# Optimization experiments

Hardware: AMD Instinct MI355X
Metric: run time of the kernel (lower is better)

## Reference

```python
import jax, jax.numpy as jnp
import numpy as np

D = 1024      # d_model
H = 16        # n_heads
HD = D // H   # head_dim = 64
B = 2
T = 2048


def setup_inputs() -> dict:
    key = jax.random.key(0)
    k0, k1, k2 = jax.random.split(key, 3)
    s = 1.0 / np.sqrt(D)
    return {
        "x": jax.random.normal(k0, (B, T, D), dtype=jnp.float32),
        "qkv_w": jax.random.normal(k1, (D, 3 * D), dtype=jnp.float32) * s,
        "qkv_b": jnp.zeros((3 * D,), dtype=jnp.float32),
        "out_w": jax.random.normal(k2, (D, D), dtype=jnp.float32) * s,
        "out_b": jnp.zeros((D,), dtype=jnp.float32),
    }


def _apply_rotary(x, rope):
    # Faithful to the torch apply_rotary: even/odd interleaved split of both
    # x and the [sin(freqs)|cos(freqs)] rope table.
    x1, x2 = x[..., ::2], x[..., 1::2]
    sin, cos = rope[..., ::2], rope[..., 1::2]
    return jnp.concatenate([x1 * cos - x2 * sin, x1 * sin + x2 * cos], axis=-1)


def reference(x, qkv_w, qkv_b, out_w, out_b):
    Bx, Tx, Dm = x.shape
    # QKV projection -> [3, B, H, T, HD]
    qkv = (x @ qkv_w + qkv_b).reshape(Bx, Tx, 3, H, HD).transpose(2, 0, 3, 1, 4)
    q, k, v = qkv[0], qkv[1], qkv[2]

    # Rotary table: rope = concat(sin(freqs), cos(freqs)) along last dim -> [T, HD]
    inv_freq = 1.0 / (10000.0 ** (jnp.arange(0, HD, 2, dtype=jnp.float32) / HD))
    t = jnp.arange(Tx, dtype=jnp.float32)
    freqs = t[:, None] * inv_freq[None, :]          # [T, HD/2]
    rope = jnp.concatenate([jnp.sin(freqs), jnp.cos(freqs)], axis=-1)  # [T, HD]

    q = _apply_rotary(q, rope)
    k = _apply_rotary(k, rope)

    scale = HD ** -0.5
    scores = jnp.einsum('bhqd,bhkd->bhqk', q, k) * scale  # [B,H,T,T]
    causal_mask = jnp.triu(jnp.ones((Tx, Tx), dtype=bool), 1)
    scores = jnp.where(causal_mask, -jnp.inf, scores)
    attn = jax.nn.softmax(scores, axis=-1)
    # dropout is identity in eval mode
    out = jnp.einsum('bhqk,bhkd->bhqd', attn, v)           # [B,H,T,HD]
    out = out.transpose(0, 2, 1, 3).reshape(Bx, Tx, Dm)    # [B,T,D]
    return out @ out_w + out_b
```

## Files before the change

### kernel.cpp

```cpp
#include <hip/hip_runtime.h>

typedef unsigned short u16;
typedef __attribute__((ext_vector_type(8))) __bf16 bf16x8;
typedef __attribute__((ext_vector_type(4))) float f32x4;

#define NB 2
#define NT 2048
#define ND 1024
#define NH 16
#define HD 64

__device__ __forceinline__ float b2f(u16 u) {
  union { float f; unsigned int i; } v; v.i = ((unsigned int)u) << 16; return v.f;
}
__device__ __forceinline__ u16 f2b(float f) {
  union { float f; unsigned int i; } v; v.f = f;
  unsigned int r = (v.i + 0x7FFFu + ((v.i >> 16) & 1u)) >> 16;
  return (u16)r;
}
__device__ __forceinline__ unsigned int cvtpk(float lo, float hi) {
  unsigned int pk;
  asm("v_cvt_pk_bf16_f32 %0, %1, %2" : "=v"(pk) : "v"(lo), "v"(hi));
  return pk;
}

__device__ __forceinline__ void gload_lds16(const u16* g, u16* lds) {
  __builtin_amdgcn_global_load_lds(
      (const __attribute__((address_space(1))) unsigned int*)(g),
      (__attribute__((address_space(3))) unsigned int*)(lds),
      16, 0, 0);
}

__device__ __forceinline__ f32x4 mfma16(bf16x8 a, bf16x8 b, f32x4 c) {
  return __builtin_amdgcn_mfma_f32_16x16x32_bf16(a, b, c, 0, 0, 0);
}

template <int N>
__device__ __forceinline__ float ror16(float x) {
  return __int_as_float(__builtin_amdgcn_update_dpp(
      __float_as_int(x), __float_as_int(x), 0x120 | N, 0xF, 0xF, true));
}
__device__ __forceinline__ float rsum16(float x) {
  x += ror16<8>(x);
  x += ror16<4>(x);
  x += ror16<2>(x);
  x += ror16<1>(x);
  return x;
}

__device__ __forceinline__ float fast_sin(float a) {
  float r = a * 0.15915494309189535f;
  r -= floorf(r);
  return __builtin_amdgcn_sinf(r);
}
__device__ __forceinline__ float fast_cos(float a) {
  float r = a * 0.15915494309189535f;
  r -= floorf(r);
  return __builtin_amdgcn_cosf(r);
}

__global__ __launch_bounds__(256) void prep_inputs(
    const float* __restrict__ x, const float* __restrict__ qkv_w,
    const float* __restrict__ out_w, u16* __restrict__ xb,
    u16* __restrict__ wqkvT, u16* __restrict__ woutT,
    float* __restrict__ rtab) {
  __shared__ u16 tile[32][33];
  const int blk = blockIdx.x;
  const int tid = threadIdx.x;
  if (blk < 2048) {
    int i = (blk * 256 + tid) * 8;
#pragma unroll
    for (int j = 0; j < 8; ++j) xb[i + j] = f2b(x[i + j]);
    return;
  }
  if (blk >= 6144) {
    const float LOG1E4 = 9.210340371976184f;
    int base = (blk - 6144) * 4096 + tid * 16;
#pragma unroll
    for (int j = 0; j < 16; ++j) {
      int idx = base + j;
      int t = idx >> 6, c = idx & 63;
      float inv = __expf(-((float)(c & 31)) * (1.0f / 32.0f) * LOG1E4);
      float a = (float)t * inv;
      rtab[idx] = (c < 32) ? fast_sin(a) : fast_cos(a);
    }
    return;
  }
  const float* in; u16* out; int N; int idx;
  if (blk < 5120) { idx = blk - 2048; in = qkv_w; out = wqkvT; N = 3072; }
  else            { idx = blk - 5120; in = out_w; out = woutT; N = 1024; }
  const int nbx = N / 32;
  const int n0 = (idx % nbx) * 32, k0 = (idx / nbx) * 32;
  const int tx = tid & 31, ty = tid >> 5;
  for (int i2 = ty; i2 < 32; i2 += 8)
    tile[i2][tx] = f2b(in[(size_t)(k0 + i2) * N + n0 + tx]);
  __syncthreads();
  for (int i2 = ty; i2 < 32; i2 += 8)
    out[(size_t)(n0 + i2) * 1024 + k0 + tx] = tile[tx][i2];
}

__global__ __launch_bounds__(256, 3) void gemm64_2ph(const u16* __restrict__ A,
                                                     const u16* __restrict__ Bt,
                                                     const float* __restrict__ bias,
                                                     float* __restrict__ C,
                                                     int M, int N, int K) {
  __shared__ alignas(16) u16 As[2][4096];
  __shared__ alignas(16) u16 Bs[2][8192];
  const int tid = threadIdx.x;
  const int lane = tid & 63;
  const int wave = tid >> 6;
  const int l15 = lane & 15, quad = lane >> 4;
  const int wm = (wave >> 1) * 32, wn = (wave & 1) * 64;

  const int lin = blockIdx.y * gridDim.x + blockIdx.x;
  const int xcd = lin & 7, loc = lin >> 3;
  const int row0 = (xcd * 8 + (loc >> 3)) * 64;
  const int col0 = (loc & 7) * 128;

  const int sr = tid >> 3;
  const size_t soff = (size_t)sr * K + (size_t)((tid & 7) ^ (sr & 7)) * 8;
  const u16* Ab = A + (size_t)row0 * K;
  const u16* Bb = Bt + (size_t)col0 * K;

  const int swz0 = (quad ^ (l15 & 7)) * 8;
  const int swz1 = ((4 + quad) ^ (l15 & 7)) * 8;
  const int arow = (wm + l15) * 64;
  const int brow = (wn + l15) * 64;

  f32x4 acc[2][4] = {};
  const int NTIL = K >> 6;

#define STAGEA(buf, koff)                                                    \
  _Pragma("unroll") for (int p = 0; p < 2; ++p)                              \
      gload_lds16(Ab + (koff) + soff + (size_t)p * 32 * K,                   \
                  &As[buf][(p * 256 + tid) * 8]);
#define STAGEB(buf, koff)                                                    \
  _Pragma("unroll") for (int p = 0; p < 4; ++p)                              \
      gload_lds16(Bb + (koff) + soff + (size_t)p * 32 * K,                   \
                  &Bs[buf][(p * 256 + tid) * 8]);

  STAGEA(0, 0);
  STAGEB(0, 0);
  asm volatile("s_waitcnt vmcnt(0)");
  __builtin_amdgcn_s_barrier();
  asm volatile("" ::: "memory");

  for (int t = 0; t < NTIL; ++t) {
    const int cur = t & 1;
    if (t + 1 < NTIL) {
      STAGEA(cur ^ 1, (size_t)(t + 1) * 64);
      STAGEB(cur ^ 1, (size_t)(t + 1) * 64);
    }
    bf16x8 af[2][2], bfr[4][2];
#pragma unroll
    for (int i = 0; i < 2; ++i) {
      af[i][0] = *(const bf16x8*)&As[cur][arow + i * 1024 + swz0];
      af[i][1] = *(const bf16x8*)&As[cur][arow + i * 1024 + swz1];
    }
#pragma unroll
    for (int j = 0; j < 4; ++j) {
      bfr[j][0] = *(const bf16x8*)&Bs[cur][brow + j * 1024 + swz0];
      bfr[j][1] = *(const bf16x8*)&Bs[cur][brow + j * 1024 + swz1];
    }
    asm volatile("s_waitcnt lgkmcnt(0)");
    __builtin_amdgcn_sched_barrier(0);
#pragma unroll
    for (int i = 0; i < 2; ++i)
#pragma unroll
      for (int j = 0; j < 4; ++j) {
        acc[i][j] = mfma16(af[i][0], bfr[j][0], acc[i][j]);
        acc[i][j] = mfma16(af[i][1], bfr[j][1], acc[i][j]);
      }
    asm volatile("s_waitcnt vmcnt(0)");
    __builtin_amdgcn_s_barrier();
    asm volatile("" ::: "memory");
  }
#undef STAGEA
#undef STAGEB

#pragma unroll
  for (int j = 0; j < 4; ++j) {
    const int c = col0 + wn + j * 16 + l15;
    const float bv = bias[c];
#pragma unroll
    for (int i = 0; i < 2; ++i) {
      const int rr0 = row0 + wm + i * 16 + quad * 4;
      f32x4 v = acc[i][j];
#pragma unroll
      for (int rr = 0; rr < 4; ++rr)
        C[(size_t)(rr0 + rr) * N + c] = v[rr] + bv;
    }
  }
}

__device__ __forceinline__ void stage2(const u16* g0, const u16* g1, u16* l,
                                       int tid) {
  gload_lds16(g0, &l[tid * 8]);
  gload_lds16(g1, &l[(512 + tid) * 8]);
}

__device__ __forceinline__ u16* tsw(u16* base, int row, int col) {
  int byte = row * 512 + ((col * 2) ^ ((row & 15) << 4));
  return (u16*)((char*)base + byte);
}

#define AH(b, h) (&lds[((b) * 2 + (h)) * 8192])
#define BH(b, h) (&lds[32768 + ((b) * 2 + (h)) * 8192])

#define LOAD_AFX(dst, base)                                                 \
  _Pragma("unroll") for (int mm = 0; mm < 4; ++mm) {                        \
    dst[mm][0] = *(const bf16x8*)&(base)[arow + mm * 2048 + swz0];          \
    dst[mm][1] = *(const bf16x8*)&(base)[arow + mm * 2048 + swz1];          \
  }
#define LOAD_BF(base)                                                       \
  _Pragma("unroll") for (int nn = 0; nn < 2; ++nn) {                        \
    bfr[nn][0] = *(const bf16x8*)&(base)[brow + nn * 4096 + swz0];          \
    bfr[nn][1] = *(const bf16x8*)&(base)[brow + nn * 4096 + swz1];          \
  }
#define MFMA_QX(afv, MA, NQ)                                                \
  _Pragma("unroll") for (int mm = 0; mm < 4; ++mm)                          \
  _Pragma("unroll") for (int nn = 0; nn < 2; ++nn) {                        \
    acc[(MA) * 4 + mm][(NQ) * 2 + nn] =                                     \
        mfma16(afv[mm][0], bfr[nn][0], acc[(MA) * 4 + mm][(NQ) * 2 + nn]);  \
    acc[(MA) * 4 + mm][(NQ) * 2 + nn] =                                     \
        mfma16(afv[mm][1], bfr[nn][1], acc[(MA) * 4 + mm][(NQ) * 2 + nn]);  \
  }
#define PH_SYNC                                                             \
  __builtin_amdgcn_s_barrier();                                             \
  asm volatile("s_waitcnt lgkmcnt(0)");                                     \
  __builtin_amdgcn_sched_barrier(0);                                        \
  __builtin_amdgcn_s_setprio(1);
#define PH_END                                                              \
  __builtin_amdgcn_s_setprio(0);                                            \
  __builtin_amdgcn_s_barrier();                                             \
  asm volatile("" ::: "memory");

__global__ __launch_bounds__(512, 2) void gemm256_qkv(const u16* __restrict__ A,
                                                      const u16* __restrict__ Bt,
                                                      const float* __restrict__ bias,
                                                      u16* __restrict__ qsw,
                                                      u16* __restrict__ ksw,
                                                      u16* __restrict__ vsw,
                                                      const float* __restrict__ rope_tab,
                                                      int K) {
  __shared__ alignas(16) u16 lds[65536];
  const int tid = threadIdx.x;
  const int lane = tid & 63;
  const int wave = tid >> 6;
  const int l15 = lane & 15, quad = lane >> 4;
  const int wm = wave >> 2, wn = wave & 3;

  const int lin = blockIdx.y * gridDim.x + blockIdx.x;
  const int xcd = lin & 7, loc = lin >> 3;
  const int row0 = ((xcd & 3) * 4 + loc / 6) * 256;
  const int col0 = ((xcd >> 2) * 6 + loc % 6) * 256;
  const int NTIL = K >> 6;

  const int sr = tid >> 3;
  const size_t soff = (size_t)sr * K + (size_t)((tid & 7) ^ (sr & 7)) * 8;
  const size_t hK = (size_t)64 * K;
  const u16* A0p = A + (size_t)row0 * K + soff;
  const u16* A1p = A0p + 2 * hK;
  const u16* B0p = Bt + (size_t)col0 * K + soff;
  const u16* B1p = B0p + 2 * hK;

  const int swz0 = (quad ^ (l15 & 7)) * 8;
  const int swz1 = ((4 + quad) ^ (l15 & 7)) * 8;
  const int arow = (wm * 16 + l15) * 64;
  const int brow = (wn * 16 + l15) * 64;

  f32x4 acc[8][4] = {};

  stage2(B0p, B0p + hK, BH(0, 0), tid);
  stage2(A1p, A1p + hK, AH(0, 1), tid);
  stage2(A0p, A0p + hK, AH(0, 0), tid);
  stage2(B1p, B1p + hK, BH(0, 1), tid);
  {
    int tp = (NTIL > 1) ? 1 : 0;
    stage2(B0p + tp * 64, B0p + tp * 64 + hK, BH(1, 0), tid);
    stage2(A1p + tp * 64, A1p + tp * 64 + hK, AH(1, 1), tid);
  }
  asm volatile("s_waitcnt vmcnt(4)");
  __builtin_amdgcn_s_barrier();
  asm volatile("" ::: "memory");

  bf16x8 afA[4][2], afB[4][2], bfr[2][2];
#pragma unroll 2
  for (int t = 0; t < NTIL; ++t) {
    const int cur = t & 1, nxt = cur ^ 1;
    const int o1 = ((t + 1 < NTIL) ? t + 1 : NTIL - 1) * 64;
    const int o2 = ((t + 2 < NTIL) ? t + 2 : NTIL - 1) * 64;
    u16* Ac0 = AH(cur, 0);
    u16* Ac1 = AH(cur, 1);
    u16* Bc0 = BH(cur, 0);
    u16* Bc1 = BH(cur, 1);

    LOAD_AFX(afA, Ac0);
    LOAD_BF(Bc0);
    stage2(A0p + o1, A0p + o1 + hK, AH(nxt, 0), tid);
    PH_SYNC; MFMA_QX(afA, 0, 0); PH_END;

    LOAD_AFX(afB, Ac1);
    stage2(B1p + o1, B1p + o1 + hK, BH(nxt, 1), tid);
    PH_SYNC; MFMA_QX(afB, 1, 0); PH_END;

    LOAD_BF(Bc1);
    stage2(B0p + o2, B0p + o2 + hK, Bc0, tid);
    PH_SYNC; MFMA_QX(afB, 1, 1); PH_END;

    stage2(A1p + o2, A1p + o2 + hK, Ac1, tid);
    __builtin_amdgcn_s_barrier();
    __builtin_amdgcn_sched_barrier(0);
    __builtin_amdgcn_s_setprio(1);
    MFMA_QX(afA, 0, 1);
    __builtin_amdgcn_s_setprio(0);
    asm volatile("s_waitcnt vmcnt(4)");
    __builtin_amdgcn_s_barrier();
    asm volatile("" ::: "memory");
  }
  asm volatile("s_waitcnt vmcnt(0)");
  __syncthreads();

#pragma unroll
  for (int ni = 0; ni < 4; ++ni) {
    const int col_in = (ni >> 1) * 128 + (ni & 1) * 64 + wn * 16 + l15;
    const float bv = bias[col0 + col_in];
#pragma unroll
    for (int mi = 0; mi < 8; ++mi) {
      const int r_in0 = (mi >> 2) * 128 + (mi & 3) * 32 + wm * 16 + quad * 4;
      f32x4 v = acc[mi][ni];
#pragma unroll
      for (int rr = 0; rr < 4; ++rr)
        *tsw(lds, r_in0 + rr, col_in) = f2b(v[rr] + bv);
    }
  }
  __syncthreads();

  const int tt = col0 >> 10;
  const int h0 = (col0 & 1023) >> 6;
  const int bb = row0 >> 11;
  const int tb0 = row0 & 2047;

  if (tt < 2) {
    u16* dst = (tt == 0) ? qsw : ksw;
    const float scale = (tt == 0) ? 0.125f : 1.0f;
    const int hh = tid >> 7;
    const int chunk = (tid >> 4) & 7;
    const int tl = tid & 15;
    const int ks = chunk >> 2, qd = chunk & 3;
    const int bh = bb * 16 + h0 + hh;
    const bool low = (ks == 0);
    const int cbase = qd * 16;
    const int xbyte0 = (hh * 64 + cbase) * 2;
    const int sw = tl << 4;
    for (int tb = 0; tb < 8; ++tb) {
      const int tbt = tb0 + tb * 32;
#pragma unroll
      for (int rbloc = 0; rbloc < 2; ++rbloc) {
        const int rrow = tb * 32 + rbloc * 16 + tl;
        const int tg = tbt + rbloc * 16 + tl;
        const char* rowp = (const char*)lds + rrow * 512;
        bf16x8 q0 = *(const bf16x8*)(rowp + (xbyte0 ^ sw));
        bf16x8 q1 = *(const bf16x8*)(rowp + ((xbyte0 + 16) ^ sw));
        const float* tp = &rope_tab[tg * 64 + cbase];
        float sc[16];
        *(f32x4*)&sc[0]  = *(const f32x4*)(tp);
        *(f32x4*)&sc[4]  = *(const f32x4*)(tp + 4);
        *(f32x4*)&sc[8]  = *(const f32x4*)(tp + 8);
        *(f32x4*)&sc[12] = *(const f32x4*)(tp + 12);
        u16 xs[16];
        *(bf16x8*)&xs[0] = q0;
        *(bf16x8*)&xs[8] = q1;
        union { u16 s[8]; unsigned int u[4]; bf16x8 v; } o;
        float ovv[8];
#pragma unroll
        for (int e = 0; e < 8; ++e) {
          float x1 = b2f(xs[2 * e]), x2 = b2f(xs[2 * e + 1]);
          float sA = sc[2 * e], cA = sc[2 * e + 1];
          float ov = low ? (x1 * cA - x2 * sA) : (x1 * sA + x2 * cA);
          ovv[e] = ov * scale;
        }
#pragma unroll
        for (int p2 = 0; p2 < 4; ++p2)
          o.u[p2] = cvtpk(ovv[2 * p2], ovv[2 * p2 + 1]);
        size_t addr =
            ((((size_t)bh * 128 + (tbt >> 4) + rbloc) * 2 + ks) * 64 +
             qd * 16 + tl) * 8;
        *(bf16x8*)&dst[addr] = o.v;
      }
    }
  } else {
    const int u = tid >> 8;
    const int utid = tid & 255;
    const int ni = utid >> 6, lane2 = utid & 63;
    const int qd = lane2 >> 4, l15b = lane2 & 15;
    for (int it = 0; it < 16; ++it) {
      const int unit = it * 2 + u;
      const int hh = unit >> 3, tb = unit & 7;
      const int bh = bb * 16 + h0 + hh;
      const int tbt = tb0 + tb * 32;
      union { u16 s[8]; bf16x8 v; } o;
#pragma unroll
      for (int e = 0; e < 8; ++e) {
        int p = qd * 8 + e;
        int krow = (p >> 1) + ((p & 1) << 4);
        o.s[e] = *tsw(lds, tb * 32 + krow, hh * 64 + ni * 16 + l15b);
      }
      *(bf16x8*)&vsw[(((size_t)bh * 64 + (tbt >> 5)) * 4 + ni) * 512 +
                     lane2 * 8] = o.v;
    }
  }
}

__global__ __launch_bounds__(128, 2) void flash_kernel(const u16* __restrict__ qsw,
                                                       const u16* __restrict__ ksw,
                                                       const u16* __restrict__ vsw,
                                                       u16* __restrict__ attn) {
  __shared__ alignas(16) u16 Ps[2 * 5120];
  float* const Of = (float*)&Ps[5120];
  float* const Ll = (float*)&Ps[9216];

  const int tid = threadIdx.x;
  const int w = tid >> 6;
  const int lane = tid & 63;
  const int l15 = lane & 15, quad = lane >> 4;
  const int linear = (int)blockIdx.x;
  const int bh = linear & 31;
  const int qt = 63 - (linear >> 5);
  const int r0 = qt * 32;
  u16* Psw = &Ps[w * 5120];

  bf16x8 aq[2][2];
#pragma unroll
  for (int mi = 0; mi < 2; ++mi)
#pragma unroll
    for (int ks = 0; ks < 2; ++ks)
      aq[mi][ks] = *(const bf16x8*)&qsw[
          ((((size_t)bh * 128 + qt * 2 + mi) * 2 + ks) * 64 + lane) * 8];

  f32x4 oacc[2][4] = {};
  float lst[8] = {0.f, 0.f, 0.f, 0.f, 0.f, 0.f, 0.f, 0.f};

  const int ktmax = qt >> 2;
  for (int kt = w; kt <= ktmax; kt += 2) {
    bf16x8 kf[2][8];
#pragma unroll
    for (int ks = 0; ks < 2; ++ks)
#pragma unroll
      for (int ni = 0; ni < 8; ++ni)
        kf[ks][ni] = *(const bf16x8*)&ksw[
            ((((size_t)bh * 128 + kt * 8 + ni) * 2 + ks) * 64 + lane) * 8];

    f32x4 sacc[2][8] = {};
#pragma unroll
    for (int ks = 0; ks < 2; ++ks)
#pragma unroll
      for (int ni = 0; ni < 8; ++ni) {
        sacc[0][ni] = mfma16(aq[0][ks], kf[ks][ni], sacc[0][ni]);
        sacc[1][ni] = mfma16(aq[1][ks], kf[ks][ni], sacc[1][ni]);
      }

    bf16x8 vf[4][4];
#pragma unroll
    for (int ks = 0; ks < 4; ++ks)
#pragma unroll
      for (int ni = 0; ni < 4; ++ni)
        vf[ks][ni] = *(const bf16x8*)&vsw[
            (((size_t)bh * 64 + kt * 4 + ks) * 4 + ni) * 512 + lane * 8];

    const bool diag = (kt == ktmax);
    const int k0 = kt * 128;
#pragma unroll
    for (int mi = 0; mi < 2; ++mi)
#pragma unroll
      for (int r = 0; r < 4; ++r) {
        const int prow = mi * 16 + quad * 4 + r;
        float sv[8];
#pragma unroll
        for (int ni = 0; ni < 8; ++ni) sv[ni] = sacc[mi][ni][r];
        if (diag) {
#pragma unroll
          for (int ni = 0; ni < 8; ++ni)
            if (k0 + ni * 16 + l15 > r0 + prow) sv[ni] = -__builtin_inff();
        }
        float rs = 0.f;
#pragma unroll
        for (int ni = 0; ni < 8; ++ni) {
          float p = __expf(sv[ni]);
          sv[ni] = p;
          rs += p;
        }
        lst[mi * 4 + r] += rsum16(rs);
#pragma unroll
        for (int ni = 0; ni < 8; ni += 2) {
          unsigned int pk = cvtpk(sv[ni], sv[ni + 1]);
          *(unsigned int*)&Psw[(ni >> 1) * 1280 + prow * 40 + 2 * l15] = pk;
        }
      }

    asm volatile("" ::: "memory");

#pragma unroll
    for (int ks = 0; ks < 4; ++ks) {
      bf16x8 ap0 = *(const bf16x8*)&Psw[ks * 1280 + l15 * 40 + quad * 8];
      bf16x8 ap1 = *(const bf16x8*)&Psw[ks * 1280 + (16 + l15) * 40 + quad * 8];
#pragma unroll
      for (int ni = 0; ni < 4; ++ni) {
        oacc[0][ni] = mfma16(ap0, vf[ks][ni], oacc[0][ni]);
        oacc[1][ni] = mfma16(ap1, vf[ks][ni], oacc[1][ni]);
      }
    }
  }

  if (w == 1) {
#pragma unroll
    for (int mi = 0; mi < 2; ++mi)
#pragma unroll
      for (int r = 0; r < 4; ++r) {
        const int row = mi * 16 + quad * 4 + r;
        if (l15 == 0) Ll[row] = lst[mi * 4 + r];
#pragma unroll
        for (int ni = 0; ni < 4; ++ni)
          Of[row * 64 + ni * 16 + l15] = oacc[mi][ni][r];
      }
  }
  __syncthreads();
  if (w == 0) {
    const int b = bh >> 4, h = bh & 15;
#pragma unroll
    for (int mi = 0; mi < 2; ++mi)
#pragma unroll
      for (int r = 0; r < 4; ++r) {
        const int row = mi * 16 + quad * 4 + r;
        const float rl = 1.0f / (lst[mi * 4 + r] + Ll[row]);
        const int trow = r0 + row;
#pragma unroll
        for (int ni = 0; ni < 4; ++ni) {
          float o = oacc[mi][ni][r] + Of[row * 64 + ni * 16 + l15];
          attn[((size_t)b * NT + trow) * ND + h * HD + ni * 16 + l15] = f2b(o * rl);
        }
      }
  }
}

extern "C" void kernel_launch(void* const* d_in, const int* in_sizes, int n_in,
                              void* d_out, int out_size, void* d_ws, size_t ws_size,
                              hipStream_t stream) {
  const float* x = (const float*)d_in[0];
  const float* qkv_w = (const float*)d_in[1];
  const float* qkv_b = (const float*)d_in[2];
  const float* out_w = (const float*)d_in[3];
  const float* out_b = (const float*)d_in[4];
  float* out = (float*)d_out;

  u16* ws = (u16*)d_ws;
  u16* xb    = ws;
  u16* wqkvT = xb + (size_t)4096 * 1024;
  u16* woutT = wqkvT + 3072 * 1024;
  u16* qsw   = woutT + 1024 * 1024;
  u16* ksw   = qsw + (size_t)32 * 2048 * 64;
  u16* vsw   = ksw + (size_t)32 * 2048 * 64;
  u16* attn  = vsw + (size_t)32 * 2048 * 64;
  float* rtab = (float*)(attn + (size_t)4096 * 1024);

  prep_inputs<<<dim3(6176), 256, 0, stream>>>(
      x, qkv_w, out_w, xb, wqkvT, woutT, rtab);

  gemm256_qkv<<<dim3(12, 16), 512, 0, stream>>>(
      xb, wqkvT, qkv_b, qsw, ksw, vsw, rtab, ND);

  flash_kernel<<<dim3(2048), 128, 0, stream>>>(qsw, ksw, vsw, attn);

  gemm64_2ph<<<dim3(ND / 128, NB * NT / 64), 256, 0, stream>>>(
      attn, woutT, out_b, out, NB * NT, ND, ND);
}
```

Measured before the change: 179.0 us.

## Replace 256x256 QKV GEMM with simpler 128x128 double-buffered tile kernel

The QKV projection moves from a 256x256 tile, 512-thread kernel with a hand-staged four-phase pipeline to a 128x128 tile, 256-thread kernel with plain double buffering and a single MFMA block per K-step. The grid grows from 192 to 768 blocks, which fills the 256 CUs more evenly than 192 blocks did. The cost is lower operand reuse per tile, more global and LDS traffic, and less overlap between loads and MFMA because each iteration waits on vmcnt(0). The epilogue's rope and V-scatter loops are resized to the smaller tile.

Result: no change. 181.5 us (+1.4%).

```diff
diff --git a/kernel.cpp b/kernel.cpp
--- a/kernel.cpp
+++ b/kernel.cpp
@@ -193,145 +193,100 @@
   }
 }
 
-__device__ __forceinline__ void stage2(const u16* g0, const u16* g1, u16* l,
-                                       int tid) {
-  gload_lds16(g0, &l[tid * 8]);
-  gload_lds16(g1, &l[(512 + tid) * 8]);
-}
-
-__device__ __forceinline__ u16* tsw(u16* base, int row, int col) {
-  int byte = row * 512 + ((col * 2) ^ ((row & 15) << 4));
+__device__ __forceinline__ u16* tsw128(u16* base, int row, int col) {
+  int byte = row * 256 + ((col * 2) ^ ((row & 15) << 4));
   return (u16*)((char*)base + byte);
 }
 
-#define AH(b, h) (&lds[((b) * 2 + (h)) * 8192])
-#define BH(b, h) (&lds[32768 + ((b) * 2 + (h)) * 8192])
-
-#define LOAD_AFX(dst, base)                                                 \
-  _Pragma("unroll") for (int mm = 0; mm < 4; ++mm) {                        \
-    dst[mm][0] = *(const bf16x8*)&(base)[arow + mm * 2048 + swz0];          \
-    dst[mm][1] = *(const bf16x8*)&(base)[arow + mm * 2048 + swz1];          \
-  }
-#define LOAD_BF(base)                                                       \
-  _Pragma("unroll") for (int nn = 0; nn < 2; ++nn) {                        \
-    bfr[nn][0] = *(const bf16x8*)&(base)[brow + nn * 4096 + swz0];          \
-    bfr[nn][1] = *(const bf16x8*)&(base)[brow + nn * 4096 + swz1];          \
-  }
-#define MFMA_QX(afv, MA, NQ)                                                \
-  _Pragma("unroll") for (int mm = 0; mm < 4; ++mm)                          \
-  _Pragma("unroll") for (int nn = 0; nn < 2; ++nn) {                        \
-    acc[(MA) * 4 + mm][(NQ) * 2 + nn] =                                     \
-        mfma16(afv[mm][0], bfr[nn][0], acc[(MA) * 4 + mm][(NQ) * 2 + nn]);  \
-    acc[(MA) * 4 + mm][(NQ) * 2 + nn] =                                     \
-        mfma16(afv[mm][1], bfr[nn][1], acc[(MA) * 4 + mm][(NQ) * 2 + nn]);  \
-  }
-#define PH_SYNC                                                             \
-  __builtin_amdgcn_s_barrier();                                             \
-  asm volatile("s_waitcnt lgkmcnt(0)");                                     \
-  __builtin_amdgcn_sched_barrier(0);                                        \
-  __builtin_amdgcn_s_setprio(1);
-#define PH_END                                                              \
-  __builtin_amdgcn_s_setprio(0);                                            \
-  __builtin_amdgcn_s_barrier();                                             \
-  asm volatile("" ::: "memory");
-
-__global__ __launch_bounds__(512, 2) void gemm256_qkv(const u16* __restrict__ A,
-                                                      const u16* __restrict__ Bt,
-                                                      const float* __restrict__ bias,
-                                                      u16* __restrict__ qsw,
-                                                      u16* __restrict__ ksw,
-                                                      u16* __restrict__ vsw,
-                                                      const float* __restrict__ rope_tab,
-                                                      int K) {
-  __shared__ alignas(16) u16 lds[65536];
+__global__ __launch_bounds__(256, 2) void gemm_qkv128(
+    const u16* __restrict__ A, const u16* __restrict__ Bt,
+    const float* __restrict__ bias, u16* __restrict__ qsw,
+    u16* __restrict__ ksw, u16* __restrict__ vsw,
+    const float* __restrict__ rope_tab, int K) {
+  __shared__ alignas(16) u16 lds[32768];
+  u16* As0 = &lds[0];
+  u16* Bs0 = &lds[8192];
+  u16* As1 = &lds[16384];
+  u16* Bs1 = &lds[24576];
   const int tid = threadIdx.x;
   const int lane = tid & 63;
   const int wave = tid >> 6;
   const int l15 = lane & 15, quad = lane >> 4;
-  const int wm = wave >> 2, wn = wave & 3;
+  const int wm = (wave >> 1) * 64, wn = (wave & 1) * 64;
 
   const int lin = blockIdx.y * gridDim.x + blockIdx.x;
   const int xcd = lin & 7, loc = lin >> 3;
-  const int row0 = ((xcd & 3) * 4 + loc / 6) * 256;
-  const int col0 = ((xcd >> 2) * 6 + loc % 6) * 256;
+  const int row0 = ((xcd & 3) * 8 + loc / 12) * 128;
+  const int col0 = ((xcd >> 2) * 12 + loc % 12) * 128;
   const int NTIL = K >> 6;
 
   const int sr = tid >> 3;
   const size_t soff = (size_t)sr * K + (size_t)((tid & 7) ^ (sr & 7)) * 8;
-  const size_t hK = (size_t)64 * K;
-  const u16* A0p = A + (size_t)row0 * K + soff;
-  const u16* A1p = A0p + 2 * hK;
-  const u16* B0p = Bt + (size_t)col0 * K + soff;
-  const u16* B1p = B0p + 2 * hK;
+  const u16* Ab = A + (size_t)row0 * K;
+  const u16* Bb = Bt + (size_t)col0 * K;
 
   const int swz0 = (quad ^ (l15 & 7)) * 8;
   const int swz1 = ((4 + quad) ^ (l15 & 7)) * 8;
-  const int arow = (wm * 16 + l15) * 64;
-  const int brow = (wn * 16 + l15) * 64;
-
-  f32x4 acc[8][4] = {};
-
-  stage2(B0p, B0p + hK, BH(0, 0), tid);
-  stage2(A1p, A1p + hK, AH(0, 1), tid);
-  stage2(A0p, A0p + hK, AH(0, 0), tid);
-  stage2(B1p, B1p + hK, BH(0, 1), tid);
-  {
-    int tp = (NTIL > 1) ? 1 : 0;
-    stage2(B0p + tp * 64, B0p + tp * 64 + hK, BH(1, 0), tid);
-    stage2(A1p + tp * 64, A1p + tp * 64 + hK, AH(1, 1), tid);
-  }
-  asm volatile("s_waitcnt vmcnt(4)");
+  const int arow = (wm + l15) * 64;
+  const int brow = (wn + l15) * 64;
+
+  f32x4 acc[4][4] = {};
+
+#define STAGE8Q(dst, bptr, koff)                                             \
+  _Pragma("unroll") for (int p = 0; p < 4; ++p)                              \
+      gload_lds16((bptr) + (koff) + soff + (size_t)p * 32 * K,               \
+                  &(dst)[(p * 256 + tid) * 8]);
+
+  STAGE8Q(As0, Ab, 0);
+  STAGE8Q(Bs0, Bb, 0);
+  asm volatile("s_waitcnt vmcnt(0)");
   __builtin_amdgcn_s_barrier();
   asm volatile("" ::: "memory");
 
-  bf16x8 afA[4][2], afB[4][2], bfr[2][2];
-#pragma unroll 2
   for (int t = 0; t < NTIL; ++t) {
-    const int cur = t & 1, nxt = cur ^ 1;
-    const int o1 = ((t + 1 < NTIL) ? t + 1 : NTIL - 1) * 64;
-    const int o2 = ((t + 2 < NTIL) ? t + 2 : NTIL - 1) * 64;
-    u16* Ac0 = AH(cur, 0);
-    u16* Ac1 = AH(cur, 1);
-    u16* Bc0 = BH(cur, 0);
-    u16* Bc1 = BH(cur, 1);
-
-    LOAD_AFX(afA, Ac0);
-    LOAD_BF(Bc0);
-    stage2(A0p + o1, A0p + o1 + hK, AH(nxt, 0), tid);
-    PH_SYNC; MFMA_QX(afA, 0, 0); PH_END;
-
-    LOAD_AFX(afB, Ac1);
-    stage2(B1p + o1, B1p + o1 + hK, BH(nxt, 1), tid);
-    PH_SYNC; MFMA_QX(afB, 1, 0); PH_END;
-
-    LOAD_BF(Bc1);
-    stage2(B0p + o2, B0p + o2 + hK, Bc0, tid);
-    PH_SYNC; MFMA_QX(afB, 1, 1); PH_END;
-
-    stage2(A1p + o2, A1p + o2 + hK, Ac1, tid);
-    __builtin_amdgcn_s_barrier();
+    u16* Ac = (t & 1) ? As1 : As0;
+    u16* Bc = (t & 1) ? Bs1 : Bs0;
+    if (t + 1 < NTIL) {
+      u16* An = (t & 1) ? As0 : As1;
+      u16* Bn = (t & 1) ? Bs0 : Bs1;
+      STAGE8Q(An, Ab, (size_t)(t + 1) * 64);
+      STAGE8Q(Bn, Bb, (size_t)(t + 1) * 64);
+    }
+    bf16x8 af[4][2], bfr[4][2];
+#pragma unroll
+    for (int i = 0; i < 4; ++i) {
+      af[i][0]  = *(const bf16x8*)&Ac[arow + i * 1024 + swz0];
+      af[i][1]  = *(const bf16x8*)&Ac[arow + i * 1024 + swz1];
+      bfr[i][0] = *(const bf16x8*)&Bc[brow + i * 1024 + swz0];
+      bfr[i][1] = *(const bf16x8*)&Bc[brow + i * 1024 + swz1];
+    }
+    asm volatile("s_waitcnt lgkmcnt(0)");
     __builtin_amdgcn_sched_barrier(0);
-    __builtin_amdgcn_s_setprio(1);
-    MFMA_QX(afA, 0, 1);
-    __builtin_amdgcn_s_setprio(0);
-    asm volatile("s_waitcnt vmcnt(4)");
+#pragma unroll
+    for (int i = 0; i < 4; ++i)
+#pragma unroll
+      for (int j = 0; j < 4; ++j) {
+        acc[i][j] = mfma16(af[i][0], bfr[j][0], acc[i][j]);
+        acc[i][j] = mfma16(af[i][1], bfr[j][1], acc[i][j]);
+      }
+    asm volatile("s_waitcnt vmcnt(0)");
     __builtin_amdgcn_s_barrier();
     asm volatile("" ::: "memory");
   }
-  asm volatile("s_waitcnt vmcnt(0)");
+#undef STAGE8Q
+
   __syncthreads();
-
-#pragma unroll
-  for (int ni = 0; ni < 4; ++ni) {
-    const int col_in = (ni >> 1) * 128 + (ni & 1) * 64 + wn * 16 + l15;
+#pragma unroll
+  for (int j = 0; j < 4; ++j) {
+    const int col_in = wn + j * 16 + l15;
     const float bv = bias[col0 + col_in];
 #pragma unroll
-    for (int mi = 0; mi < 8; ++mi) {
-      const int r_in0 = (mi >> 2) * 128 + (mi & 3) * 32 + wm * 16 + quad * 4;
-      f32x4 v = acc[mi][ni];
+    for (int i = 0; i < 4; ++i) {
+      const int r_in0 = wm + i * 16 + quad * 4;
+      f32x4 v = acc[i][j];
 #pragma unroll
       for (int rr = 0; rr < 4; ++rr)
-        *tsw(lds, r_in0 + rr, col_in) = f2b(v[rr] + bv);
+        *tsw128(lds, r_in0 + rr, col_in) = f2b(v[rr] + bv);
     }
   }
   __syncthreads();
@@ -353,13 +308,13 @@
     const int cbase = qd * 16;
     const int xbyte0 = (hh * 64 + cbase) * 2;
     const int sw = tl << 4;
-    for (int tb = 0; tb < 8; ++tb) {
+    for (int tb = 0; tb < 4; ++tb) {
       const int tbt = tb0 + tb * 32;
 #pragma unroll
       for (int rbloc = 0; rbloc < 2; ++rbloc) {
         const int rrow = tb * 32 + rbloc * 16 + tl;
         const int tg = tbt + rbloc * 16 + tl;
-        const char* rowp = (const char*)lds + rrow * 512;
+        const char* rowp = (const char*)lds + rrow * 256;
         bf16x8 q0 = *(const bf16x8*)(rowp + (xbyte0 ^ sw));
         bf16x8 q1 = *(const bf16x8*)(rowp + ((xbyte0 + 16) ^ sw));
         const float* tp = &rope_tab[tg * 64 + cbase];
@@ -390,13 +345,10 @@
       }
     }
   } else {
-    const int u = tid >> 8;
-    const int utid = tid & 255;
-    const int ni = utid >> 6, lane2 = utid & 63;
+    const int ni = tid >> 6, lane2 = tid & 63;
     const int qd = lane2 >> 4, l15b = lane2 & 15;
-    for (int it = 0; it < 16; ++it) {
-      const int unit = it * 2 + u;
-      const int hh = unit >> 3, tb = unit & 7;
+    for (int unit = 0; unit < 8; ++unit) {
+      const int hh = unit >> 2, tb = unit & 3;
       const int bh = bb * 16 + h0 + hh;
       const int tbt = tb0 + tb * 32;
       union { u16 s[8]; bf16x8 v; } o;
@@ -404,7 +356,7 @@
       for (int e = 0; e < 8; ++e) {
         int p = qd * 8 + e;
         int krow = (p >> 1) + ((p & 1) << 4);
-        o.s[e] = *tsw(lds, tb * 32 + krow, hh * 64 + ni * 16 + l15b);
+        o.s[e] = *tsw128(lds, tb * 32 + krow, hh * 64 + ni * 16 + l15b);
       }
       *(bf16x8*)&vsw[(((size_t)bh * 64 + (tbt >> 5)) * 4 + ni) * 512 +
                      lane2 * 8] = o.v;
@@ -566,7 +518,7 @@
   prep_inputs<<<dim3(6176), 256, 0, stream>>>(
       x, qkv_w, out_w, xb, wqkvT, woutT, rtab);
 
-  gemm256_qkv<<<dim3(12, 16), 512, 0, stream>>>(
+  gemm_qkv128<<<dim3(24, 32), 256, 0, stream>>>(
       xb, wqkvT, qkv_b, qsw, ksw, vsw, rtab, ND);
 
   flash_kernel<<<dim3(2048), 128, 0, stream>>>(qsw, ksw, vsw, attn);
```
